# Kernel optimization log

Measured on AMD Instinct MI355X. Metric: run time of the kernel, lower is better.

Reference implementation:

```python
import jax, jax.numpy as jnp
import numpy as np

WSCALE = 0.05  # keep ReLU MLP activations in a sane range


def setup_inputs() -> dict:
    key = jax.random.key(0)
    ks = jax.random.split(key, 9)
    B, D, H = 2048, 64, 512
    return {
        "x": jax.random.normal(ks[0], (B, D), dtype=jnp.float32),
        "W1": jax.random.normal(ks[1], (H, D), dtype=jnp.float32) * WSCALE,
        "b1": jax.random.normal(ks[2], (H,), dtype=jnp.float32) * WSCALE,
        "W2": jax.random.normal(ks[3], (H, H), dtype=jnp.float32) * WSCALE,
        "b2": jax.random.normal(ks[4], (H,), dtype=jnp.float32) * WSCALE,
        "W3": jax.random.normal(ks[5], (H, H), dtype=jnp.float32) * WSCALE,
        "b3": jax.random.normal(ks[6], (H,), dtype=jnp.float32) * WSCALE,
        "W4": jax.random.normal(ks[7], (D, H), dtype=jnp.float32) * WSCALE,
        "b4": jax.random.normal(ks[8], (D,), dtype=jnp.float32) * WSCALE,
    }


def reference(x, W1, b1, W2, b2, W3, b3, W4, b4):
    # Score network: ReLU MLP (weights stored PyTorch-style [out, in]).
    a1 = x @ W1.T + b1          # [B, H]
    h1 = jax.nn.relu(a1)
    a2 = h1 @ W2.T + b2
    h2 = jax.nn.relu(a2)
    a3 = h2 @ W3.T + b3
    h3 = jax.nn.relu(a3)
    s = h3 @ W4.T + b4          # [B, D] score

    # Divergence = trace of Jacobian ds/dx per sample.
    # Per-sample J = W4 @ diag(m3) @ W3 @ diag(m2) @ W2 @ diag(m1) @ W1,
    # with m_k = 1[a_k > 0] (ReLU derivative; 0 at 0 like torch autograd).
    m1 = (a1 > 0).astype(x.dtype)
    m2 = (a2 > 0).astype(x.dtype)
    m3 = (a3 > 0).astype(x.dtype)
    T = m1[:, :, None] * W1[None, :, :]                 # [B, H, D]
    T = m2[:, :, None] * jnp.einsum('ij,bjd->bid', W2, T)  # [B, H, D]
    T = m3[:, :, None] * jnp.einsum('ij,bjd->bid', W3, T)  # [B, H, D]
    div = jnp.einsum('dj,bjd->b', W4, T)                # trace of J, [B]

    # Hyvarinen score: 0.5 * ||s||^2 + div
    val = 0.5 * jnp.sum(s * s, axis=1) + div
    return val
```

## Files before the change

kernel.cpp:

```cpp
#include <hip/hip_runtime.h>
#include <stdint.h>


typedef __attribute__((ext_vector_type(8))) short short8;
typedef __attribute__((ext_vector_type(4))) float f32x4;

union U16x8 {
  uint4 u;
  short8 s;
};

__device__ __forceinline__ uint16_t f2bf(float f) {
  uint32_t u = __float_as_uint(f);
  uint32_t lsb = (u >> 16) & 1u;
  u += 0x7FFFu + lsb;
  return (uint16_t)(u >> 16);
}

__device__ __forceinline__ void lds_load16(const uint4* gsrc, uint4* ldst) {
  __builtin_amdgcn_global_load_lds(
      (const __attribute__((address_space(1))) void*)gsrc,
      (__attribute__((address_space(3))) void*)ldst, 16, 0, 0);
}

__global__ __launch_bounds__(256) void convert_kernel(
    const float* __restrict__ W1, const float* __restrict__ W2,
    const float* __restrict__ W3, const float* __restrict__ W4,
    uint16_t* __restrict__ A2swz, uint16_t* __restrict__ A3swz,
    uint16_t* __restrict__ B1swz, uint16_t* __restrict__ B4swz,
    float* __restrict__ W2Tf, float* __restrict__ W3Tf,
    float* __restrict__ W1Tf, float* __restrict__ W4Tf) {
  const int i = blockIdx.x * 256 + threadIdx.x;
  if (i < 262144) {
    const int e = i;
    const int f = e >> 3, j = e & 7;
    const int lane = f & 63, fk = f >> 6;
    const int kc = fk & 15, r16 = fk >> 4;
    const int l15 = lane & 15, quad = lane >> 4;
    const int row = r16 * 16 + l15, col = kc * 32 + quad * 8 + j;
    A2swz[e] = f2bf(W2[row * 512 + col]);
  } else if (i < 524288) {
    const int e = i - 262144;
    const int f = e >> 3, j = e & 7;
    const int lane = f & 63, fk = f >> 6;
    const int kc = fk & 15, r16 = fk >> 4;
    const int l15 = lane & 15, quad = lane >> 4;
    const int row = r16 * 16 + l15, col = kc * 32 + quad * 8 + j;
    A3swz[e] = f2bf(W3[col * 512 + row]);
  } else if (i < 557056) {
    const int e = i - 524288;
    const int f = e >> 3, j = e & 7;
    const int lane = f & 63, fk = f >> 6;
    const int kc = fk >> 2, jt = fk & 3;
    const int l15 = lane & 15, quad = lane >> 4;
    const int d = jt * 16 + l15, col = kc * 32 + quad * 8 + j;
    B1swz[e] = f2bf(W1[col * 64 + d]);
  } else if (i < 589824) {
    const int e = i - 557056;
    const int f = e >> 3, j = e & 7;
    const int lane = f & 63, fk = f >> 6;
    const int kc = fk >> 2, jt = fk & 3;
    const int l15 = lane & 15, quad = lane >> 4;
    const int d = jt * 16 + l15, col = kc * 32 + quad * 8 + j;
    B4swz[e] = f2bf(W4[d * 512 + col]);
  } else if (i < 851968) {
    const int e = i - 589824;
    const int k = e >> 9, jj = e & 511;
    W2Tf[e] = W2[jj * 512 + k];
  } else if (i < 1114112) {
    const int e = i - 851968;
    const int k = e >> 9, jj = e & 511;
    W3Tf[e] = W3[jj * 512 + k];
  } else if (i < 1146880) {
    const int e = i - 1114112;
    const int k = e >> 9, jj = e & 511;
    W1Tf[e] = W1[jj * 64 + k];
  } else if (i < 1179648) {
    const int e = i - 1146880;
    const int k = e >> 6, d = e & 63;
    W4Tf[e] = W4[d * 512 + k];
  }
}

__device__ __forceinline__ void fma8x4(float acc[8][4], const float w[8],
                                       const float4 h) {
#pragma unroll
  for (int p = 0; p < 8; ++p) {
    acc[p][0] = fmaf(w[p], h.x, acc[p][0]);
    acc[p][1] = fmaf(w[p], h.y, acc[p][1]);
    acc[p][2] = fmaf(w[p], h.z, acc[p][2]);
    acc[p][3] = fmaf(w[p], h.w, acc[p][3]);
  }
}

template <int KPW>
__device__ __forceinline__ void fwd_layer9(
    const float* __restrict__ WT, const float* __restrict__ bias,
    const float4* __restrict__ src, float4* __restrict__ dst,
    float4 (* __restrict__ pah)[512], uint32_t* __restrict__ mbase,
    int t, int lane, int wv) {
  float acc[8][4];
#pragma unroll
  for (int p = 0; p < 8; ++p)
#pragma unroll
    for (int s = 0; s < 4; ++s) acc[p][s] = 0.f;

  const int k0 = wv * KPW;
  const float* Wb = WT + (size_t)k0 * 512 + lane;
  float w0[8], w1[8], w2[8], w3[8];
#pragma unroll
  for (int p = 0; p < 8; ++p) {
    w0[p] = Wb[(size_t)0 * 512 + p * 64];
    w1[p] = Wb[(size_t)1 * 512 + p * 64];
    w2[p] = Wb[(size_t)2 * 512 + p * 64];
    w3[p] = Wb[(size_t)3 * 512 + p * 64];
  }
  float4 h0 = src[k0 + 0], h1 = src[k0 + 1], h2 = src[k0 + 2], h3 = src[k0 + 3];

#pragma unroll 1
  for (int kk = 0; kk < KPW; kk += 4) {
    fma8x4(acc, w0, h0);
    h0 = src[k0 + kk + 4];
#pragma unroll
    for (int p = 0; p < 8; ++p) w0[p] = Wb[(size_t)(kk + 4) * 512 + p * 64];
    fma8x4(acc, w1, h1);
    h1 = src[k0 + kk + 5];
#pragma unroll
    for (int p = 0; p < 8; ++p) w1[p] = Wb[(size_t)(kk + 5) * 512 + p * 64];
    fma8x4(acc, w2, h2);
    h2 = src[k0 + kk + 6];
#pragma unroll
    for (int p = 0; p < 8; ++p) w2[p] = Wb[(size_t)(kk + 6) * 512 + p * 64];
    fma8x4(acc, w3, h3);
    h3 = src[k0 + kk + 7];
#pragma unroll
    for (int p = 0; p < 8; ++p) w3[p] = Wb[(size_t)(kk + 7) * 512 + p * 64];
  }

  const int half = wv >> 1;
  if ((wv & 1) == 0) {
#pragma unroll
    for (int p = 0; p < 8; ++p) {
      float4 v;
      v.x = acc[p][0]; v.y = acc[p][1]; v.z = acc[p][2]; v.w = acc[p][3];
      pah[half][p * 64 + lane] = v;
    }
  }
  __syncthreads();
  if (wv & 1) {
#pragma unroll
    for (int p = 0; p < 8; ++p) {
      float4 v = pah[half][p * 64 + lane];
      v.x += acc[p][0]; v.y += acc[p][1]; v.z += acc[p][2]; v.w += acc[p][3];
      pah[half][p * 64 + lane] = v;
    }
  }
  __syncthreads();

  {
    const int u = t;
    const float4 a0 = pah[0][u], a1 = pah[1][u], a2 = pah[2][u], a3 = pah[3][u];
    const float bj = bias[u];
    float a[4];
    a[0] = ((a0.x + a1.x) + (a2.x + a3.x)) + bj;
    a[1] = ((a0.y + a1.y) + (a2.y + a3.y)) + bj;
    a[2] = ((a0.z + a1.z) + (a2.z + a3.z)) + bj;
    a[3] = ((a0.w + a1.w) + (a2.w + a3.w)) + bj;
#pragma unroll
    for (int s = 0; s < 4; ++s) {
      const unsigned long long bal = __ballot(a[s] > 0.f);
      if (lane == 0) {
        uint2 w2v;
        w2v.x = (uint32_t)bal;
        w2v.y = (uint32_t)(bal >> 32);
        *(uint2*)(mbase + (size_t)s * 16 + 2 * wv) = w2v;
      }
    }
    float4 r;
    r.x = a[0] > 0.f ? a[0] : 0.f;
    r.y = a[1] > 0.f ? a[1] : 0.f;
    r.z = a[2] > 0.f ? a[2] : 0.f;
    r.w = a[3] > 0.f ? a[3] : 0.f;
    dst[u] = r;
  }
  __syncthreads();
}

__global__ __launch_bounds__(512, 4) void forward_kernel(
    const float* __restrict__ x,
    const float* __restrict__ W1Tf, const float* __restrict__ b1,
    const float* __restrict__ W2Tf, const float* __restrict__ b2,
    const float* __restrict__ W3Tf, const float* __restrict__ b3,
    const float* __restrict__ W4Tf, const float* __restrict__ b4,
    uint32_t* __restrict__ m1p, uint32_t* __restrict__ m2p,
    uint32_t* __restrict__ m3p, float* __restrict__ out) {
  __shared__ float4 xs[64];
  __shared__ float4 hU[512];
  __shared__ float4 hV[512];
  __shared__ float4 pah[4][512];
  const int t = threadIdx.x;
  const int lane = t & 63, wv = t >> 6;
  const int b0 = blockIdx.x * 4;

  if (t < 256) {
    const int k2 = t >> 2, s2 = t & 3;
    ((float*)&xs[k2])[s2] = x[(size_t)(b0 + s2) * 64 + k2];
  }
  __syncthreads();

  fwd_layer9<8>(W1Tf, b1, xs, hU, pah, m1p + (size_t)b0 * 16, t, lane, wv);
  fwd_layer9<64>(W2Tf, b2, hU, hV, pah, m2p + (size_t)b0 * 16, t, lane, wv);
  fwd_layer9<64>(W3Tf, b3, hV, hU, pah, m3p + (size_t)b0 * 16, t, lane, wv);

  {
    const int d = lane;
    const int k0 = wv * 64;
    const float* Wb4 = W4Tf + (size_t)k0 * 64 + d;
    float a4[4] = {0.f, 0.f, 0.f, 0.f};
    float v0 = Wb4[(size_t)0 * 64], v1 = Wb4[(size_t)1 * 64];
    float v2 = Wb4[(size_t)2 * 64], v3 = Wb4[(size_t)3 * 64];
    float4 g0 = hU[k0 + 0], g1 = hU[k0 + 1], g2 = hU[k0 + 2], g3 = hU[k0 + 3];
#pragma unroll 1
    for (int kk = 0; kk < 64; kk += 4) {
      a4[0] = fmaf(v0, g0.x, a4[0]); a4[1] = fmaf(v0, g0.y, a4[1]);
      a4[2] = fmaf(v0, g0.z, a4[2]); a4[3] = fmaf(v0, g0.w, a4[3]);
      g0 = hU[k0 + kk + 4];
      v0 = Wb4[(size_t)(kk + 4) * 64];
      a4[0] = fmaf(v1, g1.x, a4[0]); a4[1] = fmaf(v1, g1.y, a4[1]);
      a4[2] = fmaf(v1, g1.z, a4[2]); a4[3] = fmaf(v1, g1.w, a4[3]);
      g1 = hU[k0 + kk + 5];
      v1 = Wb4[(size_t)(kk + 5) * 64];
      a4[0] = fmaf(v2, g2.x, a4[0]); a4[1] = fmaf(v2, g2.y, a4[1]);
      a4[2] = fmaf(v2, g2.z, a4[2]); a4[3] = fmaf(v2, g2.w, a4[3]);
      g2 = hU[k0 + kk + 6];
      v2 = Wb4[(size_t)(kk + 6) * 64];
      a4[0] = fmaf(v3, g3.x, a4[0]); a4[1] = fmaf(v3, g3.y, a4[1]);
      a4[2] = fmaf(v3, g3.z, a4[2]); a4[3] = fmaf(v3, g3.w, a4[3]);
      g3 = hU[k0 + kk + 7];
      v3 = Wb4[(size_t)(kk + 7) * 64];
    }
    const int half = wv >> 1;
    float4 pv;
    pv.x = a4[0]; pv.y = a4[1]; pv.z = a4[2]; pv.w = a4[3];
    if ((wv & 1) == 0) pah[half][d] = pv;
    __syncthreads();
    if (wv & 1) {
      float4 v = pah[half][d];
      v.x += pv.x; v.y += pv.y; v.z += pv.z; v.w += pv.w;
      pah[half][d] = v;
    }
    __syncthreads();
  }
  if (t < 64) {
    const float4 q0 = pah[0][t], q1 = pah[1][t], q2 = pah[2][t], q3 = pah[3][t];
    const float bj = b4[t];
    float sq[4];
    sq[0] = ((q0.x + q1.x) + (q2.x + q3.x)) + bj;
    sq[1] = ((q0.y + q1.y) + (q2.y + q3.y)) + bj;
    sq[2] = ((q0.z + q1.z) + (q2.z + q3.z)) + bj;
    sq[3] = ((q0.w + q1.w) + (q2.w + q3.w)) + bj;
#pragma unroll
    for (int s = 0; s < 4; ++s) sq[s] *= sq[s];
#pragma unroll
    for (int off = 32; off; off >>= 1) {
      sq[0] += __shfl_down(sq[0], off, 64);
      sq[1] += __shfl_down(sq[1], off, 64);
      sq[2] += __shfl_down(sq[2], off, 64);
      sq[3] += __shfl_down(sq[3], off, 64);
    }
    if (t == 0) {
      out[b0 + 0] = 0.5f * sq[0];
      out[b0 + 1] = 0.5f * sq[1];
      out[b0 + 2] = 0.5f * sq[2];
      out[b0 + 3] = 0.5f * sq[3];
    }
  }
}

__device__ __forceinline__ void expand_mask(uint32_t byte8, uint32_t mk[4]) {
#pragma unroll
  for (int i = 0; i < 4; ++i) {
    mk[i] = (((byte8 >> (2 * i)) & 1u) ? 0x0000FFFFu : 0u) |
            (((byte8 >> (2 * i + 1)) & 1u) ? 0xFFFF0000u : 0u);
  }
}

__global__ __launch_bounds__(512, 4) void div_kernel(
    const uint4* __restrict__ A2swz, const uint4* __restrict__ A3swz,
    const uint4* __restrict__ B1swz, const uint4* __restrict__ B4swz,
    const uint32_t* __restrict__ m1p, const uint32_t* __restrict__ m2p,
    const uint32_t* __restrict__ m3p, float* __restrict__ out) {
  __shared__ uint4 sfrag[3][16][64];
  __shared__ uint4 emask[8][16][4];
  const int t = threadIdx.x;
  const int lane = t & 63, wv = t >> 6;
  const int quad = lane >> 4, l15 = lane & 15;
  const int g4 = blockIdx.x;
  const int rowB0 = blockIdx.y * 64;
  const int sLoc = wv & 3;
  const int b = g4 * 4 + sLoc;
  const int r16b = blockIdx.y * 4;
  const bool isC = (wv < 4);

  const uint4* sb = (wv < 2) ? A2swz : (wv < 4) ? B1swz : (wv < 6) ? A3swz : B4swz;

  f32x4 acc[4][4];
#pragma unroll
  for (int it = 0; it < 4; ++it)
#pragma unroll
    for (int jt = 0; jt < 4; ++jt) acc[it][jt] = (f32x4){0.f, 0.f, 0.f, 0.f};

  {
    const uint32_t* mp = (isC ? m1p : m3p) + (size_t)b * 16;
    const int kcl = lane >> 2, qd = lane & 3;
    const uint32_t word = mp[kcl];
    uint32_t mk[4];
    expand_mask((word >> (qd * 8)) & 0xFFu, mk);
    uint4 v;
    v.x = mk[0]; v.y = mk[1]; v.z = mk[2]; v.w = mk[3];
    emask[wv][kcl][qd] = v;
  }

  auto stage = [&](int sbuf, int kc) {
#pragma unroll
    for (int q = 0; q < 2; ++q) {
      const int sub = (wv & 1) * 2 + q;
      const size_t off = ((wv & 2) == 0)
          ? ((size_t)((r16b + sub) * 16 + kc) * 64 + lane)
          : ((size_t)(kc * 4 + sub) * 64 + lane);
      lds_load16(sb + off, &sfrag[sbuf][wv * 2 + q][0]);
    }
  };

  stage(0, 0);
  stage(1, 1);
  __builtin_amdgcn_sched_barrier(0);
  asm volatile("s_waitcnt vmcnt(2)" ::: "memory");
  __builtin_amdgcn_s_barrier();
  __builtin_amdgcn_sched_barrier(0);

  const int base = isC ? 0 : 8;

#pragma unroll 1
  for (int kc = 0; kc < 16; ++kc) {
    const int rb = kc % 3;
    if (kc < 14) stage((kc + 2) % 3, kc + 2);

    const uint4 mku = emask[wv][kc][quad];

    uint4 a[4], u[4];
#pragma unroll
    for (int q = 0; q < 4; ++q) {
      a[q] = sfrag[rb][base + q][lane];
      u[q] = sfrag[rb][base + 4 + q][lane];
    }

    short8 bf[4];
#pragma unroll
    for (int jt = 0; jt < 4; ++jt) {
      U16x8 uu;
      uu.u = u[jt];
      uu.u.x &= mku.x; uu.u.y &= mku.y; uu.u.z &= mku.z; uu.u.w &= mku.w;
      bf[jt] = uu.s;
    }
#pragma unroll
    for (int it = 0; it < 4; ++it) {
      U16x8 ua;
      ua.u = a[it];
      const short8 af = ua.s;
#pragma unroll
      for (int jt = 0; jt < 4; ++jt)
        acc[it][jt] = __builtin_amdgcn_mfma_f32_16x16x32_bf16(af, bf[jt], acc[it][jt], 0, 0, 0);
    }

    if (kc < 14) {
      asm volatile("s_waitcnt vmcnt(2)" ::: "memory");
    } else if (kc == 14) {
      asm volatile("s_waitcnt vmcnt(0)" ::: "memory");
    }
    if (kc < 15) {
      __builtin_amdgcn_s_barrier();
      __builtin_amdgcn_sched_barrier(0);
    }
  }

  __syncthreads();
  float* cxf = (float*)&sfrag[0][0][0];
  float dsum = 0.f;
  const uint32_t* m2w = m2p + (size_t)b * 16;
#pragma unroll
  for (int h = 0; h < 2; ++h) {
    if (isC) {
#pragma unroll
      for (int ith = 0; ith < 2; ++ith)
#pragma unroll
        for (int jt = 0; jt < 4; ++jt) {
          float* crow = &cxf[((size_t)sLoc * 32 + ith * 16 + quad * 4) * 65 +
                             jt * 16 + l15];
          crow[0 * 65] = acc[h * 2 + ith][jt][0];
          crow[1 * 65] = acc[h * 2 + ith][jt][1];
          crow[2 * 65] = acc[h * 2 + ith][jt][2];
          crow[3 * 65] = acc[h * 2 + ith][jt][3];
        }
    }
    __syncthreads();
    if (!isC) {
#pragma unroll
      for (int ith = 0; ith < 2; ++ith) {
        const int it = h * 2 + ith;
        const int rloc = it * 16 + quad * 4;
        const uint32_t md = m2w[(rowB0 + rloc) >> 5];
        const uint32_t bits = (md >> (rloc & 31)) & 0xFu;
        const float w0 = (bits & 1u) ? 1.f : 0.f;
        const float w1 = (bits & 2u) ? 1.f : 0.f;
        const float w2 = (bits & 4u) ? 1.f : 0.f;
        const float w3 = (bits & 8u) ? 1.f : 0.f;
#pragma unroll
        for (int jt = 0; jt < 4; ++jt) {
          const float* crow = &cxf[((size_t)sLoc * 32 + ith * 16 + quad * 4) * 65 +
                                   jt * 16 + l15];
          dsum = fmaf(w0, acc[it][jt][0] * crow[0 * 65], dsum);
          dsum = fmaf(w1, acc[it][jt][1] * crow[1 * 65], dsum);
          dsum = fmaf(w2, acc[it][jt][2] * crow[2 * 65], dsum);
          dsum = fmaf(w3, acc[it][jt][3] * crow[3 * 65], dsum);
        }
      }
    }
    __syncthreads();
  }
  if (!isC) {
#pragma unroll
    for (int off = 32; off; off >>= 1) dsum += __shfl_down(dsum, off, 64);
    if (lane == 0) atomicAdd(out + b, dsum);
  }
}

extern "C" void kernel_launch(void* const* d_in, const int* in_sizes, int n_in,
                              void* d_out, int out_size, void* d_ws, size_t ws_size,
                              hipStream_t stream) {
  const float* x  = (const float*)d_in[0];
  const float* W1 = (const float*)d_in[1];
  const float* b1 = (const float*)d_in[2];
  const float* W2 = (const float*)d_in[3];
  const float* b2 = (const float*)d_in[4];
  const float* W3 = (const float*)d_in[5];
  const float* b3 = (const float*)d_in[6];
  const float* W4 = (const float*)d_in[7];
  const float* b4 = (const float*)d_in[8];
  float* out = (float*)d_out;

  char* ws = (char*)d_ws;
  uint16_t* A2swz = (uint16_t*)(ws + 0);
  uint16_t* A3swz = (uint16_t*)(ws + 524288);
  uint16_t* B1swz = (uint16_t*)(ws + 1048576);
  uint16_t* B4swz = (uint16_t*)(ws + 1114112);
  float*    W2Tf  = (float*)(ws + 1179648);
  float*    W3Tf  = (float*)(ws + 2228224);
  float*    W1Tf  = (float*)(ws + 3276800);
  float*    W4Tf  = (float*)(ws + 3407872);
  uint32_t* m1p   = (uint32_t*)(ws + 3538944);
  uint32_t* m2p   = (uint32_t*)(ws + 3670016);
  uint32_t* m3p   = (uint32_t*)(ws + 3801088);
  if (ws_size < 3932160) return;

  convert_kernel<<<4608, 256, 0, stream>>>(W1, W2, W3, W4,
                                           A2swz, A3swz, B1swz, B4swz,
                                           W2Tf, W3Tf, W1Tf, W4Tf);
  forward_kernel<<<512, 512, 0, stream>>>(x, W1Tf, b1, W2Tf, b2, W3Tf, b3,
                                          W4Tf, b4, m1p, m2p, m3p, out);
  div_kernel<<<dim3(512, 8), 512, 0, stream>>>((const uint4*)A2swz,
                                               (const uint4*)A3swz,
                                               (const uint4*)B1swz,
                                               (const uint4*)B4swz,
                                               m1p, m2p, m3p, out);
}
```

Measured before the change: 263.0 us.

## Prefetch next-layer weights into cache during forward layers; split div kernel launches

Inside each forward layer's K loop, every thread issues a strided dummy load from the next layer's weight matrix so it is warm in cache when that layer starts. Separately, the divergence kernel is split into four launches over slices of blockIdx.y, presumably to improve cache locality of the swizzled weight fragments per launch. The prefetch adds extra memory traffic and loop instructions, and the split adds launch overhead and serialization between slices.

New measurement: 476.7 us. 81.3% more time.

```diff
diff --git a/kernel.cpp b/kernel.cpp
--- a/kernel.cpp
+++ b/kernel.cpp
@@ -98,7 +98,7 @@
     const float* __restrict__ WT, const float* __restrict__ bias,
     const float4* __restrict__ src, float4* __restrict__ dst,
     float4 (* __restrict__ pah)[512], uint32_t* __restrict__ mbase,
-    int t, int lane, int wv) {
+    int t, int lane, int wv, const float* __restrict__ warm, int warmN) {
   float acc[8][4];
 #pragma unroll
   for (int p = 0; p < 8; ++p)
@@ -116,6 +116,7 @@
     w3[p] = Wb[(size_t)3 * 512 + p * 64];
   }
   float4 h0 = src[k0 + 0], h1 = src[k0 + 1], h2 = src[k0 + 2], h3 = src[k0 + 3];
+  float pf = 0.f;
 
 #pragma unroll 1
   for (int kk = 0; kk < KPW; kk += 4) {
@@ -135,7 +136,15 @@
     h3 = src[k0 + kk + 7];
 #pragma unroll
     for (int p = 0; p < 8; ++p) w3[p] = Wb[(size_t)(kk + 7) * 512 + p * 64];
-  }
+    {
+      const int q = kk >> 2;
+      if (warm != nullptr && q < warmN) {
+        asm volatile("" ::"v"(pf));
+        pf = warm[((size_t)q * 512 + t) * 32];
+      }
+    }
+  }
+  asm volatile("" ::"v"(pf));
 
   const int half = wv >> 1;
   if ((wv & 1) == 0) {
@@ -208,9 +217,12 @@
   }
   __syncthreads();
 
-  fwd_layer9<8>(W1Tf, b1, xs, hU, pah, m1p + (size_t)b0 * 16, t, lane, wv);
-  fwd_layer9<64>(W2Tf, b2, hU, hV, pah, m2p + (size_t)b0 * 16, t, lane, wv);
-  fwd_layer9<64>(W3Tf, b3, hV, hU, pah, m3p + (size_t)b0 * 16, t, lane, wv);
+  fwd_layer9<8>(W1Tf, b1, xs, hU, pah, m1p + (size_t)b0 * 16, t, lane, wv,
+                W2Tf, 2);
+  fwd_layer9<64>(W2Tf, b2, hU, hV, pah, m2p + (size_t)b0 * 16, t, lane, wv,
+                 W3Tf, 16);
+  fwd_layer9<64>(W3Tf, b3, hV, hU, pah, m3p + (size_t)b0 * 16, t, lane, wv,
+                 W4Tf, 2);
 
   {
     const int d = lane;
@@ -289,17 +301,18 @@
     const uint4* __restrict__ A2swz, const uint4* __restrict__ A3swz,
     const uint4* __restrict__ B1swz, const uint4* __restrict__ B4swz,
     const uint32_t* __restrict__ m1p, const uint32_t* __restrict__ m2p,
-    const uint32_t* __restrict__ m3p, float* __restrict__ out) {
+    const uint32_t* __restrict__ m3p, float* __restrict__ out, int y0) {
   __shared__ uint4 sfrag[3][16][64];
   __shared__ uint4 emask[8][16][4];
   const int t = threadIdx.x;
   const int lane = t & 63, wv = t >> 6;
   const int quad = lane >> 4, l15 = lane & 15;
   const int g4 = blockIdx.x;
-  const int rowB0 = blockIdx.y * 64;
+  const int yb = y0 + blockIdx.y;
+  const int rowB0 = yb * 64;
   const int sLoc = wv & 3;
   const int b = g4 * 4 + sLoc;
-  const int r16b = blockIdx.y * 4;
+  const int r16b = yb * 4;
   const bool isC = (wv < 4);
 
   const uint4* sb = (wv < 2) ? A2swz : (wv < 4) ? B1swz : (wv < 6) ? A3swz : B4swz;
@@ -468,9 +481,11 @@
                                            W2Tf, W3Tf, W1Tf, W4Tf);
   forward_kernel<<<512, 512, 0, stream>>>(x, W1Tf, b1, W2Tf, b2, W3Tf, b3,
                                           W4Tf, b4, m1p, m2p, m3p, out);
-  div_kernel<<<dim3(512, 8), 512, 0, stream>>>((const uint4*)A2swz,
-                                               (const uint4*)A3swz,
-                                               (const uint4*)B1swz,
-                                               (const uint4*)B4swz,
-                                               m1p, m2p, m3p, out);
-}
+  for (int y0 = 0; y0 < 8; y0 += 2) {
+    div_kernel<<<dim3(512, 2), 512, 0, stream>>>((const uint4*)A2swz,
+                                                 (const uint4*)A3swz,
+                                                 (const uint4*)B1swz,
+                                                 (const uint4*)B4swz,
+                                                 m1p, m2p, m3p, out, y0);
+  }
+}
```

## Restructure div_kernel so each wave shares B fragments across four samples in registers

Applied to the files above, without the earlier changes.

The divergence kernel is reorganised so each wave owns one 16-row A tile and loops over the four samples in the block. The per-sample mask is now applied to the A fragment instead of B. B fragments are loaded straight from global memory into registers, and only A is double-buffered through LDS, which removes the per-iteration workgroup barrier. Launch bounds are switched to amdgpu_waves_per_eu(4,4). The intent is less LDS traffic and fewer barriers, at the cost of direct global loads of B on every iteration and a vmcnt(0) wait each step.

Measured after the change: 264.5 us. No clear change (+0.6%).

```diff
diff --git a/kernel.cpp b/kernel.cpp
--- a/kernel.cpp
+++ b/kernel.cpp
@@ -186,7 +186,9 @@
   __syncthreads();
 }
 
-__global__ __launch_bounds__(512, 4) void forward_kernel(
+__global__ __launch_bounds__(512)
+__attribute__((amdgpu_waves_per_eu(4, 4)))
+void forward_kernel(
     const float* __restrict__ x,
     const float* __restrict__ W1Tf, const float* __restrict__ b1,
     const float* __restrict__ W2Tf, const float* __restrict__ b2,
@@ -285,130 +287,127 @@
   }
 }
 
-__global__ __launch_bounds__(512, 4) void div_kernel(
+__global__ __launch_bounds__(512)
+__attribute__((amdgpu_waves_per_eu(4, 4)))
+void div_kernel(
     const uint4* __restrict__ A2swz, const uint4* __restrict__ A3swz,
     const uint4* __restrict__ B1swz, const uint4* __restrict__ B4swz,
     const uint32_t* __restrict__ m1p, const uint32_t* __restrict__ m2p,
     const uint32_t* __restrict__ m3p, float* __restrict__ out) {
-  __shared__ uint4 sfrag[3][16][64];
-  __shared__ uint4 emask[8][16][4];
+  __shared__ uint4 sfragP[2][8][64];
+  __shared__ uint4 emask2[2][4][16][4];
+  __shared__ float cxf[8 * 16 * 65];
   const int t = threadIdx.x;
   const int lane = t & 63, wv = t >> 6;
   const int quad = lane >> 4, l15 = lane & 15;
   const int g4 = blockIdx.x;
   const int rowB0 = blockIdx.y * 64;
-  const int sLoc = wv & 3;
-  const int b = g4 * 4 + sLoc;
+  const int q = wv & 3;
   const int r16b = blockIdx.y * 4;
   const bool isC = (wv < 4);
-
-  const uint4* sb = (wv < 2) ? A2swz : (wv < 4) ? B1swz : (wv < 6) ? A3swz : B4swz;
+  const int role = isC ? 0 : 1;
+
+  const uint4* sbA = isC ? A2swz : A3swz;
+  const uint4* sbB = isC ? B1swz : B4swz;
 
   f32x4 acc[4][4];
 #pragma unroll
-  for (int it = 0; it < 4; ++it)
-#pragma unroll
-    for (int jt = 0; jt < 4; ++jt) acc[it][jt] = (f32x4){0.f, 0.f, 0.f, 0.f};
+  for (int s = 0; s < 4; ++s)
+#pragma unroll
+    for (int jt = 0; jt < 4; ++jt) acc[s][jt] = (f32x4){0.f, 0.f, 0.f, 0.f};
 
   {
-    const uint32_t* mp = (isC ? m1p : m3p) + (size_t)b * 16;
+    const int r = wv >> 2, s = wv & 3;
+    const uint32_t* mp = (r == 0 ? m1p : m3p) + (size_t)(g4 * 4 + s) * 16;
     const int kcl = lane >> 2, qd = lane & 3;
     const uint32_t word = mp[kcl];
     uint32_t mk[4];
     expand_mask((word >> (qd * 8)) & 0xFFu, mk);
     uint4 v;
     v.x = mk[0]; v.y = mk[1]; v.z = mk[2]; v.w = mk[3];
-    emask[wv][kcl][qd] = v;
-  }
-
-  auto stage = [&](int sbuf, int kc) {
-#pragma unroll
-    for (int q = 0; q < 2; ++q) {
-      const int sub = (wv & 1) * 2 + q;
-      const size_t off = ((wv & 2) == 0)
-          ? ((size_t)((r16b + sub) * 16 + kc) * 64 + lane)
-          : ((size_t)(kc * 4 + sub) * 64 + lane);
-      lds_load16(sb + off, &sfrag[sbuf][wv * 2 + q][0]);
-    }
+    emask2[r][s][kcl][qd] = v;
+  }
+
+  auto stageA = [&](int sbuf, int kc) {
+    const size_t off = (size_t)((r16b + q) * 16 + kc) * 64 + lane;
+    lds_load16(sbA + off, &sfragP[sbuf][wv][0]);
   };
 
-  stage(0, 0);
-  stage(1, 1);
+  uint4 u[4];
+  stageA(0, 0);
+#pragma unroll
+  for (int jt = 0; jt < 4; ++jt) u[jt] = sbB[(size_t)jt * 64 + lane];
   __builtin_amdgcn_sched_barrier(0);
-  asm volatile("s_waitcnt vmcnt(2)" ::: "memory");
+  asm volatile("s_waitcnt vmcnt(0) lgkmcnt(0)" ::: "memory");
   __builtin_amdgcn_s_barrier();
   __builtin_amdgcn_sched_barrier(0);
 
-  const int base = isC ? 0 : 8;
-
 #pragma unroll 1
   for (int kc = 0; kc < 16; ++kc) {
-    const int rb = kc % 3;
-    if (kc < 14) stage((kc + 2) % 3, kc + 2);
-
-    const uint4 mku = emask[wv][kc][quad];
-
-    uint4 a[4], u[4];
-#pragma unroll
-    for (int q = 0; q < 4; ++q) {
-      a[q] = sfrag[rb][base + q][lane];
-      u[q] = sfrag[rb][base + 4 + q][lane];
-    }
-
-    short8 bf[4];
+    const int buf = kc & 1;
+    if (kc < 15) stageA(buf ^ 1, kc + 1);
+
+    const uint4 a1 = sfragP[buf][wv][lane];
+
+    short8 bu[4];
 #pragma unroll
     for (int jt = 0; jt < 4; ++jt) {
       U16x8 uu;
       uu.u = u[jt];
-      uu.u.x &= mku.x; uu.u.y &= mku.y; uu.u.z &= mku.z; uu.u.w &= mku.w;
-      bf[jt] = uu.s;
-    }
-#pragma unroll
-    for (int it = 0; it < 4; ++it) {
-      U16x8 ua;
-      ua.u = a[it];
-      const short8 af = ua.s;
+      bu[jt] = uu.s;
+    }
+    if (kc < 15) {
 #pragma unroll
       for (int jt = 0; jt < 4; ++jt)
-        acc[it][jt] = __builtin_amdgcn_mfma_f32_16x16x32_bf16(af, bf[jt], acc[it][jt], 0, 0, 0);
-    }
-
-    if (kc < 14) {
-      asm volatile("s_waitcnt vmcnt(2)" ::: "memory");
-    } else if (kc == 14) {
+        u[jt] = sbB[(size_t)((kc + 1) * 4 + jt) * 64 + lane];
+    }
+
+#pragma unroll
+    for (int s = 0; s < 4; ++s) {
+      const uint4 mku = emask2[role][s][kc][quad];
+      U16x8 am;
+      am.u.x = a1.x & mku.x;
+      am.u.y = a1.y & mku.y;
+      am.u.z = a1.z & mku.z;
+      am.u.w = a1.w & mku.w;
+      const short8 af = am.s;
+#pragma unroll
+      for (int jt = 0; jt < 4; ++jt)
+        acc[s][jt] = __builtin_amdgcn_mfma_f32_16x16x32_bf16(af, bu[jt], acc[s][jt], 0, 0, 0);
+    }
+
+    if (kc < 15) {
       asm volatile("s_waitcnt vmcnt(0)" ::: "memory");
-    }
-    if (kc < 15) {
-      __builtin_amdgcn_s_barrier();
       __builtin_amdgcn_sched_barrier(0);
     }
   }
 
   __syncthreads();
-  float* cxf = (float*)&sfrag[0][0][0];
-  float dsum = 0.f;
-  const uint32_t* m2w = m2p + (size_t)b * 16;
+  float dsum[4] = {0.f, 0.f, 0.f, 0.f};
 #pragma unroll
   for (int h = 0; h < 2; ++h) {
     if (isC) {
 #pragma unroll
-      for (int ith = 0; ith < 2; ++ith)
+      for (int sh = 0; sh < 2; ++sh) {
+        const int s = h * 2 + sh;
 #pragma unroll
         for (int jt = 0; jt < 4; ++jt) {
-          float* crow = &cxf[((size_t)sLoc * 32 + ith * 16 + quad * 4) * 65 +
+          float* crow = &cxf[((size_t)(q * 2 + sh) * 16 + quad * 4) * 65 +
                              jt * 16 + l15];
-          crow[0 * 65] = acc[h * 2 + ith][jt][0];
-          crow[1 * 65] = acc[h * 2 + ith][jt][1];
-          crow[2 * 65] = acc[h * 2 + ith][jt][2];
-          crow[3 * 65] = acc[h * 2 + ith][jt][3];
+          crow[0 * 65] = acc[s][jt][0];
+          crow[1 * 65] = acc[s][jt][1];
+          crow[2 * 65] = acc[s][jt][2];
+          crow[3 * 65] = acc[s][jt][3];
         }
+      }
     }
     __syncthreads();
     if (!isC) {
 #pragma unroll
-      for (int ith = 0; ith < 2; ++ith) {
-        const int it = h * 2 + ith;
-        const int rloc = it * 16 + quad * 4;
+      for (int sh = 0; sh < 2; ++sh) {
+        const int s = h * 2 + sh;
+        const uint32_t* m2w = m2p + (size_t)(g4 * 4 + s) * 16;
+        const int rloc = q * 16 + quad * 4;
         const uint32_t md = m2w[(rowB0 + rloc) >> 5];
         const uint32_t bits = (md >> (rloc & 31)) & 0xFu;
         const float w0 = (bits & 1u) ? 1.f : 0.f;
@@ -417,12 +416,12 @@
         const float w3 = (bits & 8u) ? 1.f : 0.f;
 #pragma unroll
         for (int jt = 0; jt < 4; ++jt) {
-          const float* crow = &cxf[((size_t)sLoc * 32 + ith * 16 + quad * 4) * 65 +
+          const float* crow = &cxf[((size_t)(q * 2 + sh) * 16 + quad * 4) * 65 +
                                    jt * 16 + l15];
-          dsum = fmaf(w0, acc[it][jt][0] * crow[0 * 65], dsum);
-          dsum = fmaf(w1, acc[it][jt][1] * crow[1 * 65], dsum);
-          dsum = fmaf(w2, acc[it][jt][2] * crow[2 * 65], dsum);
-          dsum = fmaf(w3, acc[it][jt][3] * crow[3 * 65], dsum);
+          dsum[s] = fmaf(w0, acc[s][jt][0] * crow[0 * 65], dsum[s]);
+          dsum[s] = fmaf(w1, acc[s][jt][1] * crow[1 * 65], dsum[s]);
+          dsum[s] = fmaf(w2, acc[s][jt][2] * crow[2 * 65], dsum[s]);
+          dsum[s] = fmaf(w3, acc[s][jt][3] * crow[3 * 65], dsum[s]);
         }
       }
     }
@@ -430,8 +429,12 @@
   }
   if (!isC) {
 #pragma unroll
-    for (int off = 32; off; off >>= 1) dsum += __shfl_down(dsum, off, 64);
-    if (lane == 0) atomicAdd(out + b, dsum);
+    for (int s = 0; s < 4; ++s) {
+      float v = dsum[s];
+#pragma unroll
+      for (int off = 32; off; off >>= 1) v += __shfl_down(v, off, 64);
+      if (lane == 0) atomicAdd(out + (g4 * 4 + s), v);
+    }
   }
 }
 
```
